# Kernel tuning notes

Measured on AMD Instinct MI355X. Metric: run time of the kernel, lower is better.

## Reference

```python
import jax, jax.numpy as jnp
import numpy as np

IN, OUT, WS = 128, 64, 512
B, H, W = 4, 128, 128
GAIN = (2.0 / (1.0 + 0.2 ** 2)) ** 0.5  # util.lrelu_gain for leaky_relu(0.2)
EPS = 1e-8


def up2_bilinear_ac(x):
    # bilinear upsample x2, align_corners=True (torch F.upsample_bilinear semantics)
    _, _, h, w = x.shape
    ys = jnp.linspace(0.0, h - 1.0, 2 * h)
    xs = jnp.linspace(0.0, w - 1.0, 2 * w)
    y0 = jnp.floor(ys).astype(jnp.int32)
    y1 = jnp.minimum(y0 + 1, h - 1)
    wy = (ys - y0).astype(x.dtype)
    x0 = jnp.floor(xs).astype(jnp.int32)
    x1 = jnp.minimum(x0 + 1, w - 1)
    wx = (xs - x0).astype(x.dtype)
    t = x[:, :, y0, :] * (1 - wy)[None, None, :, None] + x[:, :, y1, :] * wy[None, None, :, None]
    return t[:, :, :, x0] * (1 - wx) + t[:, :, :, x1] * wx


def convt3(x, w):
    # torch conv_transpose2d(stride=1, padding=1, k=3) == conv2d with spatially
    # flipped kernel, weight layout [I,O,3,3] -> lax 'IOHW' spec, SAME padding.
    wf = w[:, :, ::-1, ::-1]
    return jax.lax.conv_general_dilated(
        x, wf, (1, 1), ((1, 1), (1, 1)),
        dimension_numbers=('NCHW', 'IOHW', 'NCHW'))


def mod_conv(x, style, w, he):
    # StyleGAN2 modulate + demodulate, expressed in fused activation form:
    # y[b,o] = demod[b,o] * convT(x[b] * style[b,:,None,None], he*W)  (same math
    # as building the per-sample grouped weight tensor in the original).
    wh = w * he                                  # [I,O,3,3]
    wsq = jnp.sum(wh * wh, axis=(2, 3))          # [I,O]
    d = jax.lax.rsqrt(jnp.einsum('bi,io->bo', style * style, wsq) + EPS)  # [B,O]
    y = convt3(x * style[:, :, None, None], wh)
    return y * d[:, :, None, None] * GAIN        # forward also multiplies by gain


def setup_inputs() -> dict:
    key = jax.random.key(0)
    ks = jax.random.split(key, 16)
    f = lambda k, s: jax.random.normal(k, s, dtype=jnp.float32)
    return {
        'x': f(ks[0], (B, IN, H, W)),
        'w': f(ks[1], (B, WS, 1, 1)),
        'conv1_w': f(ks[2], (IN, OUT, 3, 3)),
        'conv2_w': f(ks[3], (OUT, OUT, 3, 3)),
        'bias1': jnp.zeros((1, OUT, 1, 1), jnp.float32),
        'bias2': jnp.zeros((1, OUT, 1, 1), jnp.float32),
        'aaff1_w': f(ks[4], (IN, WS)),
        'aaff1_b': jnp.zeros((IN,), jnp.float32),
        'aaff2_w': f(ks[5], (OUT, WS)),
        'aaff2_b': jnp.zeros((OUT,), jnp.float32),
        'baff1_w': f(ks[6], (OUT,)) * 0.1,
        'baff2_w': f(ks[7], (OUT,)) * 0.1,
        'rgb_w': f(ks[8], (3, OUT)),
        'rgb_b': jnp.zeros((3,), jnp.float32),
        'noise1': f(ks[9], (B, 1, 2 * H, 2 * W)),
        'noise2': f(ks[10], (B, 1, 2 * H, 2 * W)),
    }


def reference(x, w, conv1_w, conv2_w, bias1, bias2, aaff1_w, aaff1_b,
              aaff2_w, aaff2_b, baff1_w, baff2_w, rgb_w, rgb_b,
              noise1, noise2):
    he1 = GAIN / (IN * 9) ** 0.5
    he2 = GAIN / (OUT * 9) ** 0.5
    he_a = 1.0 / WS ** 0.5
    he_rgb = 0.03 / OUT ** 0.5

    xu = up2_bilinear_ac(x)                       # [B,IN,2H,2W]
    wv = w[:, :, 0, 0]                            # [B,WS]

    s1 = jnp.einsum('ow,bw->bo', aaff1_w * he_a, wv) + aaff1_b
    h = mod_conv(xu, s1, conv1_w, he1)
    h = h + noise1 * baff1_w[None, :, None, None] + bias1
    h = jax.nn.leaky_relu(h, 0.2)

    s2 = jnp.einsum('ow,bw->bo', aaff2_w * he_a, wv) + aaff2_b
    h = mod_conv(h, s2, conv2_w, he2)
    h = h + noise2 * baff2_w[None, :, None, None] + bias2
    h = jax.nn.leaky_relu(h, 0.2)

    rgb = jnp.einsum('oc,bchw->bohw', rgb_w * he_rgb, h) + rgb_b[None, :, None, None]
    return (h, rgb)
```

## Files before the change

### kernel.cpp

```cpp
#include <hip/hip_runtime.h>
#include <hip/hip_bf16.h>
#include <math.h>

#define BN 4
#define CIN 128
#define COUT 64
#define WSDIM 512
#define HI 128
#define WI 128
#define HO 256
#define WO 256
#define EPSC 1e-8f
#define GAINC 1.3867504905630728f
#define HE1 (GAINC/33.941125496954285f)
#define HE2 (GAINC/24.0f)
#define SUP (127.0f/255.0f)

typedef __attribute__((ext_vector_type(8))) short s16x8;
typedef __attribute__((ext_vector_type(4))) float f32x4_t;
typedef __attribute__((ext_vector_type(4))) unsigned int u32x4;

static __device__ __forceinline__ float lrelu(float v){ return v > 0.f ? v : 0.2f*v; }
static __device__ __forceinline__ unsigned short bfbits(float v){
  __hip_bfloat16 h = __float2bfloat16(v);
  return *reinterpret_cast<unsigned short*>(&h);
}
static __device__ __forceinline__ unsigned int packbf(float a, float b){
  return (unsigned int)bfbits(a) | ((unsigned int)bfbits(b) << 16);
}
static __device__ __forceinline__ void gload_lds16(const void* g, void* l){
  __builtin_amdgcn_global_load_lds(
      (const __attribute__((address_space(1))) void*)g,
      (__attribute__((address_space(3))) void*)l, 16, 0, 0);
}

__global__ __launch_bounds__(256) void k_prep(
    const float* __restrict__ w, const float* __restrict__ c1w, const float* __restrict__ c2w,
    const float* __restrict__ a1w, const float* __restrict__ a1b,
    const float* __restrict__ a2w, const float* __restrict__ a2b,
    unsigned short* __restrict__ B1, unsigned short* __restrict__ B2,
    float* __restrict__ s1, float* __restrict__ s2,
    float* __restrict__ d1g, float* __restrict__ d2g,
    unsigned int* __restrict__ zpage)
{
  const int g = blockIdx.x, t = threadIdx.x;
  __shared__ float sh1[CIN];
  __shared__ float sh2[COUT];
  if (g < 144) {
    if (g == 0 && t < 64) zpage[t] = 0u;
    int cc = g / 36, r = g - cc * 36, k = r >> 2, ot = r & 3;
    for (int e = t; e < 512; e += 256) {
      int l = e >> 3, j = e & 7;
      int c = cc * 32 + (l >> 4) * 8 + j, o = ot * 16 + (l & 15);
      B1[g * 512 + e] = bfbits(c1w[(c * COUT + o) * 9 + (8 - k)] * HE1);
    }
  } else if (g < 288) {
    int g2 = g - 144;
    int cc = g2 / 36, r = g2 - cc * 36, k = r >> 2, ot = r & 3;
    for (int e = t; e < 512; e += 256) {
      int l = e >> 3, j = e & 7;
      int c = cc * 32 + (l >> 4) * 8 + j, o = ot * 16 + (l & 15);
      B2[g2 * 512 + e] = bfbits(c2w[(c * COUT + o) * 9 + (8 - k)] * HE2);
    }
  } else {
    const int b = g - 288;
    const float he_a = 0.044194173824159216f;
    const float* wv = w + b * WSDIM;
    if (t < CIN) {
      float acc = 0.f;
      const float* ap = a1w + t * WSDIM;
      for (int k = 0; k < WSDIM; ++k) acc += ap[k] * wv[k];
      float v = acc * he_a + a1b[t];
      sh1[t] = v; s1[b * CIN + t] = v;
    } else if (t < CIN + COUT) {
      int o = t - CIN;
      float acc = 0.f;
      const float* ap = a2w + o * WSDIM;
      for (int k = 0; k < WSDIM; ++k) acc += ap[k] * wv[k];
      float v = acc * he_a + a2b[o];
      sh2[o] = v; s2[b * COUT + o] = v;
    }
    __syncthreads();
    const int o = t >> 2, p = t & 3;
    float acc = 0.f;
    for (int c = p * 32; c < p * 32 + 32; ++c) {
      const float* wp = c1w + (size_t)(c * COUT + o) * 9;
      float ws_ = 0.f;
      #pragma unroll
      for (int k = 0; k < 9; ++k) ws_ += wp[k] * wp[k];
      acc += sh1[c] * sh1[c] * ws_;
    }
    acc += __shfl_xor(acc, 1); acc += __shfl_xor(acc, 2);
    if (p == 0) d1g[b * COUT + o] = rsqrtf(acc * HE1 * HE1 + EPSC) * GAINC;
    float ac2 = 0.f;
    for (int c = p * 16; c < p * 16 + 16; ++c) {
      const float* wp = c2w + (size_t)(c * COUT + o) * 9;
      float ws_ = 0.f;
      #pragma unroll
      for (int k = 0; k < 9; ++k) ws_ += wp[k] * wp[k];
      ac2 += sh2[c] * sh2[c] * ws_;
    }
    ac2 += __shfl_xor(ac2, 1); ac2 += __shfl_xor(ac2, 2);
    if (p == 0) d2g[b * COUT + o] = rsqrtf(ac2 * HE2 * HE2 + EPSC) * GAINC;
  }
}

__global__ __launch_bounds__(256) void k_conv1(
    const float* __restrict__ x, const unsigned short* __restrict__ B1pre,
    const float* __restrict__ s1, const float* __restrict__ noise1,
    const float* __restrict__ bias1, const float* __restrict__ baff1,
    const float* __restrict__ d1g, const float* __restrict__ s2,
    unsigned short* __restrict__ h1)
{
  const int id = blockIdx.x;
  const int swz = (id & 7) * 128 + (id >> 3);
  const int b = swz >> 8;
  const int oy0 = ((swz >> 4) & 15) * 16, ox0 = (swz & 15) * 16;
  const int tid = threadIdx.x;
  const int lane = tid & 63, wv = tid >> 6;
  const int lx = lane & 15, lg = lane >> 4;

  __shared__ __align__(16) float patch[11 * 12 * 36];
  __shared__ __align__(16) unsigned int ldsA[324 * 16];
  __shared__ float s1L[CIN];

  const int ty = oy0 > 0 ? oy0 - 1 : 0;
  const int tx = ox0 > 0 ? ox0 - 1 : 0;
  const int py0 = min((ty * 127) / 255, HI - 11);
  const int px0 = min((tx * 127) / 255, WI - 12);

  if (tid < CIN) s1L[tid] = s1[b * CIN + tid];

  f32x4_t acc[4][4];
  #pragma unroll
  for (int i = 0; i < 4; ++i)
    #pragma unroll
    for (int j = 0; j < 4; ++j) acc[i][j] = (f32x4_t){0.f, 0.f, 0.f, 0.f};

  float pr[5][4];
  auto PLOAD = [&](int cc) {
    #pragma unroll
    for (int i = 0; i < 5; ++i) {
      int u = tid + i * 256;
      if (u < 1056) {
        int pair = u / 3, part = u - pair * 3;
        int ch = pair & 31, r = pair >> 5;
        const float* src = x + (((size_t)b * CIN + cc * 32 + ch) << 14)
                             + (py0 + r) * WI + px0 + part * 4;
        pr[i][0] = src[0]; pr[i][1] = src[1]; pr[i][2] = src[2]; pr[i][3] = src[3];
      }
    }
  };
  auto PSTORE = [&](int cc) {
    #pragma unroll
    for (int i = 0; i < 5; ++i) {
      int u = tid + i * 256;
      if (u < 1056) {
        int pair = u / 3, part = u - pair * 3;
        int ch = pair & 31, r = pair >> 5;
        float sv = s1L[cc * 32 + ch];
        float* dst = &patch[(r * 12 + part * 4) * 36 + ch];
        dst[0] = pr[i][0] * sv; dst[36] = pr[i][1] * sv;
        dst[72] = pr[i][2] * sv; dst[108] = pr[i][3] * sv;
      }
    }
  };

  const s16x8* Bb = (const s16x8*)B1pre;

  PLOAD(0);
  for (int cc = 0; cc < 4; ++cc) {
    __syncthreads();
    PSTORE(cc);
    __syncthreads();
    if (cc < 3) PLOAD(cc + 1);
    for (int e = tid; e < 1296; e += 256) {
      int pos = e >> 2, q = e & 3;
      int ys = pos / 18, xs = pos - ys * 18;
      int yy = oy0 - 1 + ys, xx = ox0 - 1 + xs;
      u32x4 outv = {0u, 0u, 0u, 0u};
      if (yy >= 0 && yy < HO && xx >= 0 && xx < WO) {
        float fy = yy * SUP; int y0 = (int)fy; float wy = fy - (float)y0;
        float fx = xx * SUP; int x0 = (int)fx; float wx = fx - (float)x0;
        int r0 = y0 - py0, r1 = min(y0 + 1, HI - 1) - py0;
        int c0 = x0 - px0, c1 = min(x0 + 1, WI - 1) - px0;
        const float* p00 = &patch[(r0 * 12 + c0) * 36 + q * 8];
        const float* p01 = &patch[(r0 * 12 + c1) * 36 + q * 8];
        const float* p10 = &patch[(r1 * 12 + c0) * 36 + q * 8];
        const float* p11 = &patch[(r1 * 12 + c1) * 36 + q * 8];
        unsigned int pk[4];
        #pragma unroll
        for (int h = 0; h < 2; ++h) {
          f32x4_t a00 = *(const f32x4_t*)(p00 + h * 4);
          f32x4_t a01 = *(const f32x4_t*)(p01 + h * 4);
          f32x4_t a10 = *(const f32x4_t*)(p10 + h * 4);
          f32x4_t a11 = *(const f32x4_t*)(p11 + h * 4);
          float v[4];
          #pragma unroll
          for (int j = 0; j < 4; ++j) {
            float t0 = a00[j] + (a10[j] - a00[j]) * wy;
            float t1 = a01[j] + (a11[j] - a01[j]) * wy;
            v[j] = t0 + (t1 - t0) * wx;
          }
          pk[h * 2 + 0] = packbf(v[0], v[1]);
          pk[h * 2 + 1] = packbf(v[2], v[3]);
        }
        outv = (u32x4){pk[0], pk[1], pk[2], pk[3]};
      }
      *(u32x4*)(ldsA + pos * 16 + q * 4) = outv;
    }
    __syncthreads();
    #pragma unroll
    for (int k = 0; k < 9; ++k) {
      const int dy = k / 3, dx = k - 3 * (k / 3);
      s16x8 b0 = Bb[((cc * 9 + k) * 4 + 0) * 64 + lane];
      s16x8 b1 = Bb[((cc * 9 + k) * 4 + 1) * 64 + lane];
      s16x8 b2 = Bb[((cc * 9 + k) * 4 + 2) * 64 + lane];
      s16x8 b3 = Bb[((cc * 9 + k) * 4 + 3) * 64 + lane];
      #pragma unroll
      for (int yi = 0; yi < 4; ++yi) {
        int row = (wv * 4 + yi + dy) * 18 + (lx + dx);
        s16x8 a = *(const s16x8*)((const char*)ldsA + (size_t)row * 64 + lg * 16);
        acc[yi][0] = __builtin_amdgcn_mfma_f32_16x16x32_bf16(a, b0, acc[yi][0], 0, 0, 0);
        acc[yi][1] = __builtin_amdgcn_mfma_f32_16x16x32_bf16(a, b1, acc[yi][1], 0, 0, 0);
        acc[yi][2] = __builtin_amdgcn_mfma_f32_16x16x32_bf16(a, b2, acc[yi][2], 0, 0, 0);
        acc[yi][3] = __builtin_amdgcn_mfma_f32_16x16x32_bf16(a, b3, acc[yi][3], 0, 0, 0);
      }
    }
  }
  #pragma unroll
  for (int yi = 0; yi < 4; ++yi) {
    int y = oy0 + wv * 4 + yi;
    f32x4_t nv = *(const f32x4_t*)(noise1 + (size_t)b * HO * WO + (size_t)y * WO + ox0 + lg * 4);
    #pragma unroll
    for (int ot = 0; ot < 4; ++ot) {
      int o = ot * 16 + lx;
      float d = d1g[b * COUT + o], ba = baff1[o], bi = bias1[o], sv = s2[b * COUT + o];
      #pragma unroll
      for (int jj = 0; jj < 4; ++jj) {
        float v = acc[yi][ot][jj] * d + nv[jj] * ba + bi;
        v = lrelu(v) * sv;
        int xg = ox0 + lg * 4 + jj;
        h1[(((size_t)b * HO + y) * WO + xg) * COUT + o] = bfbits(v);
      }
    }
  }
}

__global__ __launch_bounds__(256) void k_conv2(
    const unsigned short* __restrict__ h1, const unsigned short* __restrict__ B2pre,
    const float* __restrict__ noise2, const float* __restrict__ bias2, const float* __restrict__ baff2,
    const float* __restrict__ d2g, const float* __restrict__ rgbw, const float* __restrict__ rgbb,
    const unsigned int* __restrict__ zpage,
    float* __restrict__ hout, float* __restrict__ rgbout)
{
  const int id = blockIdx.x;
  const int swz = (id & 7) * 128 + (id >> 3);
  const int b = swz >> 8;
  const int oy0 = ((swz >> 4) & 15) * 16, ox0 = (swz & 15) * 16;
  const int tid = threadIdx.x;
  const int lane = tid & 63, wv = tid >> 6;
  const int lx = lane & 15, lg = lane >> 4;

  __shared__ __align__(16) unsigned int ldsA[2][1536 * 4];

  f32x4_t acc[4][4];
  #pragma unroll
  for (int i = 0; i < 4; ++i)
    #pragma unroll
    for (int j = 0; j < 4; ++j) acc[i][j] = (f32x4_t){0.f, 0.f, 0.f, 0.f};

  const s16x8* Bb = (const s16x8*)B2pre;

  const int e0u = __builtin_amdgcn_readfirstlane(tid & ~63);
  #pragma unroll
  for (int cc = 0; cc < 2; ++cc) {
    #pragma unroll
    for (int i = 0; i < 6; ++i) {
      int ebase = i * 256 + e0u;
      int e = ebase + lane;
      int pos = e >> 2, q = e & 3;
      int ys = pos / 18, xs = pos - ys * 18;
      int yy = oy0 - 1 + ys, xx = ox0 - 1 + xs;
      bool ok = (e < 1296) && (yy >= 0) && (yy < HO) && (xx >= 0) && (xx < WO);
      const void* src = ok
          ? (const void*)(h1 + ((((size_t)b * HO + yy) * WO + xx) * COUT) + cc * 32 + q * 8)
          : (const void*)zpage;
      gload_lds16(src, (void*)&ldsA[cc][(size_t)ebase * 4]);
    }
  }
  __syncthreads();

  #pragma unroll
  for (int cc = 0; cc < 2; ++cc) {
    const char* bufc = (const char*)ldsA[cc];
    #pragma unroll
    for (int k = 0; k < 9; ++k) {
      const int dy = k / 3, dx = k - 3 * (k / 3);
      s16x8 b0 = Bb[((cc * 9 + k) * 4 + 0) * 64 + lane];
      s16x8 b1 = Bb[((cc * 9 + k) * 4 + 1) * 64 + lane];
      s16x8 b2 = Bb[((cc * 9 + k) * 4 + 2) * 64 + lane];
      s16x8 b3 = Bb[((cc * 9 + k) * 4 + 3) * 64 + lane];
      #pragma unroll
      for (int yi = 0; yi < 4; ++yi) {
        int row = (wv * 4 + yi + dy) * 18 + (lx + dx);
        s16x8 a = *(const s16x8*)(bufc + (size_t)row * 64 + lg * 16);
        acc[yi][0] = __builtin_amdgcn_mfma_f32_16x16x32_bf16(a, b0, acc[yi][0], 0, 0, 0);
        acc[yi][1] = __builtin_amdgcn_mfma_f32_16x16x32_bf16(a, b1, acc[yi][1], 0, 0, 0);
        acc[yi][2] = __builtin_amdgcn_mfma_f32_16x16x32_bf16(a, b2, acc[yi][2], 0, 0, 0);
        acc[yi][3] = __builtin_amdgcn_mfma_f32_16x16x32_bf16(a, b3, acc[yi][3], 0, 0, 0);
      }
    }
  }
  const float her = 0.03f / 8.0f;
  #pragma unroll
  for (int yi = 0; yi < 4; ++yi) {
    int y = oy0 + wv * 4 + yi;
    f32x4_t nv = *(const f32x4_t*)(noise2 + (size_t)b * HO * WO + (size_t)y * WO + ox0 + lg * 4);
    float r[3][4];
    #pragma unroll
    for (int ch = 0; ch < 3; ++ch)
      #pragma unroll
      for (int jj = 0; jj < 4; ++jj) r[ch][jj] = 0.f;
    #pragma unroll
    for (int ot = 0; ot < 4; ++ot) {
      int o = ot * 16 + lx;
      float d = d2g[b * COUT + o], ba = baff2[o], bi = bias2[o];
      float w0 = rgbw[o], w1 = rgbw[COUT + o], w2 = rgbw[2 * COUT + o];
      f32x4_t hv;
      #pragma unroll
      for (int jj = 0; jj < 4; ++jj) {
        float v = acc[yi][ot][jj] * d + nv[jj] * ba + bi;
        v = lrelu(v);
        hv[jj] = v;
        r[0][jj] += w0 * v; r[1][jj] += w1 * v; r[2][jj] += w2 * v;
      }
      *(f32x4_t*)(hout + ((size_t)(b * COUT + o) * HO + y) * WO + ox0 + lg * 4) = hv;
    }
    #pragma unroll
    for (int ch = 0; ch < 3; ++ch)
      #pragma unroll
      for (int jj = 0; jj < 4; ++jj) {
        float s = r[ch][jj];
        s += __shfl_xor(s, 1); s += __shfl_xor(s, 2);
        s += __shfl_xor(s, 4); s += __shfl_xor(s, 8);
        r[ch][jj] = s;
      }
    if (lx < 12) {
      float val = 0.f;
      #pragma unroll
      for (int ii = 0; ii < 12; ++ii) if (lx == ii) val = r[ii >> 2][ii & 3];
      int ch = lx >> 2, jj = lx & 3;
      rgbout[(((size_t)(b * 3 + ch)) * HO + y) * WO + ox0 + lg * 4 + jj] = val * her + rgbb[ch];
    }
  }
}

extern "C" void kernel_launch(void* const* d_in, const int* in_sizes, int n_in,
                              void* d_out, int out_size, void* d_ws, size_t ws_size,
                              hipStream_t stream) {
  const float* x      = (const float*)d_in[0];
  const float* w      = (const float*)d_in[1];
  const float* c1w    = (const float*)d_in[2];
  const float* c2w    = (const float*)d_in[3];
  const float* bias1  = (const float*)d_in[4];
  const float* bias2  = (const float*)d_in[5];
  const float* a1w    = (const float*)d_in[6];
  const float* a1b    = (const float*)d_in[7];
  const float* a2w    = (const float*)d_in[8];
  const float* a2b    = (const float*)d_in[9];
  const float* baff1  = (const float*)d_in[10];
  const float* baff2  = (const float*)d_in[11];
  const float* rgbw   = (const float*)d_in[12];
  const float* rgbb   = (const float*)d_in[13];
  const float* noise1 = (const float*)d_in[14];
  const float* noise2 = (const float*)d_in[15];

  const size_t h1_bytes = (size_t)BN * HO * WO * COUT * 2;
  unsigned short* h1 = (unsigned short*)d_ws;
  char* p = (char*)d_ws + h1_bytes;
  float* s1  = (float*)p;               p += BN * CIN * 4;
  float* s2  = (float*)p;               p += BN * COUT * 4;
  float* d1g = (float*)p;               p += BN * COUT * 4;
  float* d2g = (float*)p;               p += BN * COUT * 4;
  unsigned short* B1pre = (unsigned short*)p;  p += 144 * 512 * 2;
  unsigned short* B2pre = (unsigned short*)p;  p += 144 * 512 * 2;
  unsigned int* zpage = (unsigned int*)p;

  float* hout   = (float*)d_out;
  float* rgbout = hout + (size_t)BN * COUT * HO * WO;

  k_prep<<<292, 256, 0, stream>>>(w, c1w, c2w, a1w, a1b, a2w, a2b, B1pre, B2pre, s1, s2, d1g, d2g, zpage);
  k_conv1<<<1024, 256, 0, stream>>>(x, B1pre, s1, noise1, bias1, baff1, d1g, s2, h1);
  k_conv2<<<1024, 256, 0, stream>>>(h1, B2pre, noise2, bias2, baff2, d2g, rgbw, rgbb, zpage, hout, rgbout);
}
```

Baseline: 138.7 us.

## Stage conv1 input patch with direct global-to-LDS loads overlapped with MFMA

```diff
diff --git a/kernel.cpp b/kernel.cpp
--- a/kernel.cpp
+++ b/kernel.cpp
@@ -120,14 +120,15 @@
   const int lane = tid & 63, wv = tid >> 6;
   const int lx = lane & 15, lg = lane >> 4;
 
-  __shared__ __align__(16) float patch[11 * 12 * 36];
-  __shared__ __align__(16) unsigned int ldsA[324 * 16];
+  __shared__ __align__(16) float patch[5632];
+  __shared__ __align__(16) unsigned int ldsA[1296 * 4];
   __shared__ float s1L[CIN];
 
   const int ty = oy0 > 0 ? oy0 - 1 : 0;
   const int tx = ox0 > 0 ? ox0 - 1 : 0;
   const int py0 = min((ty * 127) / 255, HI - 11);
   const int px0 = min((tx * 127) / 255, WI - 12);
+  const int px0a = px0 & ~3;
 
   if (tid < CIN) s1L[tid] = s1[b * CIN + tid];
 
@@ -137,43 +138,34 @@
     #pragma unroll
     for (int j = 0; j < 4; ++j) acc[i][j] = (f32x4_t){0.f, 0.f, 0.f, 0.f};
 
-  float pr[5][4];
-  auto PLOAD = [&](int cc) {
+  auto STAGE = [&](int cc) {
+    const float* xb = x + (((size_t)b * CIN + cc * 32) << 14);
     #pragma unroll
     for (int i = 0; i < 5; ++i) {
-      int u = tid + i * 256;
-      if (u < 1056) {
-        int pair = u / 3, part = u - pair * 3;
-        int ch = pair & 31, r = pair >> 5;
-        const float* src = x + (((size_t)b * CIN + cc * 32 + ch) << 14)
-                             + (py0 + r) * WI + px0 + part * 4;
-        pr[i][0] = src[0]; pr[i][1] = src[1]; pr[i][2] = src[2]; pr[i][3] = src[3];
-      }
+      int ub = i * 256 + (wv << 6);
+      int u = ub + lane;
+      int ch = u / 44, rem = u - ch * 44;
+      int rr = rem >> 2, ck = rem & 3;
+      int col = min(px0a + ck * 4, 124);
+      const float* src = xb + ((size_t)ch << 14) + (py0 + rr) * WI + col;
+      gload_lds16((const void*)src, (void*)&patch[(size_t)ub * 4]);
+    }
+    if (wv < 2) {
+      int ub = 1280 + (wv << 6);
+      int u = ub + lane;
+      int ch = u / 44, rem = u - ch * 44;
+      int rr = rem >> 2, ck = rem & 3;
+      int col = min(px0a + ck * 4, 124);
+      const float* src = xb + ((size_t)ch << 14) + (py0 + rr) * WI + col;
+      gload_lds16((const void*)src, (void*)&patch[(size_t)ub * 4]);
     }
   };
-  auto PSTORE = [&](int cc) {
-    #pragma unroll
-    for (int i = 0; i < 5; ++i) {
-      int u = tid + i * 256;
-      if (u < 1056) {
-        int pair = u / 3, part = u - pair * 3;
-        int ch = pair & 31, r = pair >> 5;
-        float sv = s1L[cc * 32 + ch];
-        float* dst = &patch[(r * 12 + part * 4) * 36 + ch];
-        dst[0] = pr[i][0] * sv; dst[36] = pr[i][1] * sv;
-        dst[72] = pr[i][2] * sv; dst[108] = pr[i][3] * sv;
-      }
-    }
-  };
 
   const s16x8* Bb = (const s16x8*)B1pre;
 
-  PLOAD(0);
+  STAGE(0);
+  __syncthreads();
   for (int cc = 0; cc < 4; ++cc) {
-    __syncthreads();
-    PSTORE(cc);
-    __syncthreads();
-    if (cc < 3) PLOAD(cc + 1);
     for (int e = tid; e < 1296; e += 256) {
       int pos = e >> 2, q = e & 3;
       int ys = pos / 18, xs = pos - ys * 18;
@@ -183,33 +175,24 @@
         float fy = yy * SUP; int y0 = (int)fy; float wy = fy - (float)y0;
         float fx = xx * SUP; int x0 = (int)fx; float wx = fx - (float)x0;
         int r0 = y0 - py0, r1 = min(y0 + 1, HI - 1) - py0;
-        int c0 = x0 - px0, c1 = min(x0 + 1, WI - 1) - px0;
-        const float* p00 = &patch[(r0 * 12 + c0) * 36 + q * 8];
-        const float* p01 = &patch[(r0 * 12 + c1) * 36 + q * 8];
-        const float* p10 = &patch[(r1 * 12 + c0) * 36 + q * 8];
-        const float* p11 = &patch[(r1 * 12 + c1) * 36 + q * 8];
-        unsigned int pk[4];
+        int c0 = x0 - px0a;
+        float v[8];
         #pragma unroll
-        for (int h = 0; h < 2; ++h) {
-          f32x4_t a00 = *(const f32x4_t*)(p00 + h * 4);
-          f32x4_t a01 = *(const f32x4_t*)(p01 + h * 4);
-          f32x4_t a10 = *(const f32x4_t*)(p10 + h * 4);
-          f32x4_t a11 = *(const f32x4_t*)(p11 + h * 4);
-          float v[4];
-          #pragma unroll
-          for (int j = 0; j < 4; ++j) {
-            float t0 = a00[j] + (a10[j] - a00[j]) * wy;
-            float t1 = a01[j] + (a11[j] - a01[j]) * wy;
-            v[j] = t0 + (t1 - t0) * wx;
-          }
-          pk[h * 2 + 0] = packbf(v[0], v[1]);
-          pk[h * 2 + 1] = packbf(v[2], v[3]);
+        for (int j = 0; j < 8; ++j) {
+          const float* pc = &patch[(q * 8 + j) * 176];
+          float tl = pc[r0 * 16 + c0], tr = pc[r0 * 16 + c0 + 1];
+          float bl = pc[r1 * 16 + c0], br = pc[r1 * 16 + c0 + 1];
+          float t0 = tl + (bl - tl) * wy;
+          float t1 = tr + (br - tr) * wy;
+          v[j] = (t0 + (t1 - t0) * wx) * s1L[cc * 32 + q * 8 + j];
         }
-        outv = (u32x4){pk[0], pk[1], pk[2], pk[3]};
+        outv = (u32x4){packbf(v[0], v[1]), packbf(v[2], v[3]),
+                       packbf(v[4], v[5]), packbf(v[6], v[7])};
       }
       *(u32x4*)(ldsA + pos * 16 + q * 4) = outv;
     }
     __syncthreads();
+    if (cc < 3) STAGE(cc + 1);
     #pragma unroll
     for (int k = 0; k < 9; ++k) {
       const int dy = k / 3, dx = k - 3 * (k / 3);
@@ -227,6 +210,7 @@
         acc[yi][3] = __builtin_amdgcn_mfma_f32_16x16x32_bf16(a, b3, acc[yi][3], 0, 0, 0);
       }
     }
+    if (cc < 3) __syncthreads();
   }
   #pragma unroll
   for (int yi = 0; yi < 4; ++yi) {
```

New measurement: 151.0 us. +8.9%, slower.
